# Kernel optimization log

Measured on AMD Instinct MI355X. Metric: run time of the kernel, lower is better.

The kernel has to match this reference:

```python
import jax, jax.numpy as jnp
import numpy as np

N = 50000      # nodes
E = 800000     # edges (avg degree 16)
D = 128        # node_dim
H = 128        # hidden_dim
ED = 16        # edge_dim (unused by GCNConv, kept for signature fidelity)
G = 64         # graphs in batch
EPS = 1e-5     # BatchNorm eps


def setup_inputs() -> dict:
    key = jax.random.key(0)
    ks = jax.random.split(key, 16)
    s = 0.05
    inp = {
        "x": jax.random.normal(ks[0], (N, D), jnp.float32),
        "edge_index": jax.random.randint(ks[1], (2, E), 0, N, dtype=jnp.int64),
        "edge_attr": jax.random.normal(ks[2], (E, ED), jnp.float32),
        "batch": jnp.sort(jax.random.randint(ks[3], (N,), 0, G, dtype=jnp.int64)),
        # GCNConv weights/biases
        "W1": jax.random.normal(ks[4], (D, H), jnp.float32) * s,
        "b1": jnp.zeros((H,), jnp.float32),
        "W2": jax.random.normal(ks[5], (H, H), jnp.float32) * s,
        "b2": jnp.zeros((H,), jnp.float32),
        "W3": jax.random.normal(ks[6], (H, H), jnp.float32) * s,
        "b3": jnp.zeros((H,), jnp.float32),
        # BatchNorm affine params (training-mode batch stats)
        "g1": jnp.ones((H,), jnp.float32), "be1": jnp.zeros((H,), jnp.float32),
        "g2": jnp.ones((H,), jnp.float32), "be2": jnp.zeros((H,), jnp.float32),
        "g3": jnp.ones((H,), jnp.float32), "be3": jnp.zeros((H,), jnp.float32),
    }
    return inp


def reference(x, edge_index, edge_attr, batch,
              W1, b1, W2, b2, W3, b3,
              g1, be1, g2, be2, g3, be3):
    n = x.shape[0]
    src, dst = edge_index[0], edge_index[1]

    # GCN symmetric normalization with added self-loops:
    # deg[i] = 1 + in_degree(i); norm(e) = deg[src]^-1/2 * deg[dst]^-1/2
    deg = jax.ops.segment_sum(jnp.ones((src.shape[0],), x.dtype), dst,
                              num_segments=n) + 1.0
    dinv = jax.lax.rsqrt(deg)
    edge_norm = (dinv[src] * dinv[dst])[:, None]   # [E,1]
    self_norm = (dinv * dinv)[:, None]             # [N,1] self-loop weight

    def gcn(h, W, b):
        h = h @ W                                  # [N,H]
        agg = jax.ops.segment_sum(h[src] * edge_norm, dst, num_segments=n)
        return agg + h * self_norm + b

    def bn_sigmoid(h, g, b):
        m = h.mean(0)
        v = jnp.mean(jnp.square(h - m), 0)         # biased variance (torch BN)
        return jax.nn.sigmoid((h - m) * jax.lax.rsqrt(v + EPS) * g + b)

    h = bn_sigmoid(gcn(x, W1, b1), g1, be1)
    h = bn_sigmoid(gcn(h, W2, b2), g2, be2)
    h = bn_sigmoid(gcn(h, W3, b3), g3, be3)

    # global_mean_pool over graph ids
    cnt = jax.ops.segment_sum(jnp.ones((n,), h.dtype), batch, num_segments=G)
    pooled = jax.ops.segment_sum(h, batch, num_segments=G)
    return pooled / jnp.maximum(cnt, 1.0)[:, None]
```

## Files before the change

kernel.cpp:

```cpp
#include <hip/hip_runtime.h>
#include <math.h>

#define NDIM 128

typedef __attribute__((ext_vector_type(8))) short short8;
typedef __attribute__((ext_vector_type(4))) float f32x4;

__device__ __forceinline__ float sigmoidf_(float x){ return 1.0f/(1.0f + __expf(-x)); }

__device__ __forceinline__ unsigned short f2bf(float f){
  unsigned u = __float_as_uint(f);
  unsigned r = (u + 0x7fffu + ((u >> 16) & 1u)) >> 16;
  return (unsigned short)r;
}
__device__ __forceinline__ float bflo(unsigned u){ return __uint_as_float(u<<16); }
__device__ __forceinline__ float bfhi(unsigned u){ return __uint_as_float(u & 0xffff0000u); }

__global__ void pass1_k(const int* __restrict__ dst, int* __restrict__ counts,
                        int* __restrict__ rank, int E){
  int e = blockIdx.x*blockDim.x + threadIdx.x;
  if(e < E) rank[e] = atomicAdd(&counts[dst[e]], 1);
}

__global__ void scan1_k(const int* __restrict__ counts, int* __restrict__ scanned,
                        int* __restrict__ chunksums, int N){
  __shared__ int lds[256];
  int t = threadIdx.x; int idx = blockIdx.x*256 + t;
  int x = (idx < N) ? counts[idx] : 0;
  lds[t] = x; __syncthreads();
  for(int o=1;o<256;o<<=1){
    int v = (t>=o) ? lds[t-o] : 0;
    __syncthreads();
    lds[t] += v;
    __syncthreads();
  }
  if(idx < N) scanned[idx] = lds[t];
  if(t == 255) chunksums[blockIdx.x] = lds[255];
}

__global__ void scan2_k(int* __restrict__ chunksums, int nchunks){
  __shared__ int lds[256];
  int t = threadIdx.x;
  int x = (t < nchunks) ? chunksums[t] : 0;
  lds[t] = x; __syncthreads();
  for(int o=1;o<256;o<<=1){
    int v = (t>=o) ? lds[t-o] : 0;
    __syncthreads();
    lds[t] += v;
    __syncthreads();
  }
  if(t < nchunks) chunksums[t] = lds[t] - x;
}

__global__ void scan3_k(const int* __restrict__ scanned, const int* __restrict__ counts,
                        const int* __restrict__ chunksums, int* __restrict__ row_start,
                        float* __restrict__ dinv, int N){
  int i = blockIdx.x*blockDim.x + threadIdx.x;
  if(i < N){
    row_start[i] = scanned[i] - counts[i] + chunksums[i>>8];
    dinv[i] = rsqrtf(1.0f + (float)counts[i]);
  }
}

__global__ void pass2_k(const int* __restrict__ src, const int* __restrict__ dst,
                        const int* __restrict__ rank, const int* __restrict__ row_start,
                        unsigned short* __restrict__ csr, int E){
  int e = blockIdx.x*blockDim.x + threadIdx.x;
  if(e >= E) return;
  csr[row_start[dst[e]] + rank[e]] = (unsigned short)src[e];
}

__global__ void wprep_k(const float* __restrict__ W0, const float* __restrict__ W1,
                        const float* __restrict__ W2, unsigned short* __restrict__ Wsw,
                        const int* __restrict__ batch, int* __restrict__ bound,
                        int N, int G){
  int t = blockIdx.x*256 + threadIdx.x;
  if(t < 3*16384){
    int l = t >> 14; int i = t & 16383;
    const float* W = (l==0) ? W0 : ((l==1) ? W1 : W2);
    int k = i >> 7, n = i & 127;
    Wsw[l*16384 + (((k>>3)*128 + n)<<3) + (k&7)] = f2bf(W[k*128+n]);
  } else {
    int g = t - 3*16384;
    if(g <= G){
      int lo = 0, hi = N;
      while(lo < hi){ int mid = (lo+hi)>>1; if(batch[mid] < g) lo = mid+1; else hi = mid; }
      bound[g] = lo;
    }
  }
}

__global__ __launch_bounds__(256) void gemm_mfma_k(const void* __restrict__ Avoid,
                                                   const unsigned short* __restrict__ Wsw,
                                                   unsigned short* __restrict__ Bh,
                                                   const float* __restrict__ dinv,
                                                   const float* __restrict__ sums,
                                                   const float* __restrict__ sumsq,
                                                   const float* __restrict__ gam,
                                                   const float* __restrict__ bet,
                                                   int N){
  __shared__ unsigned short Al[16384];
  __shared__ unsigned short Wl[16384];
  __shared__ float scl[NDIM], shl[NDIM], dvl[NDIM];
  int t = threadIdx.x;
  int row0 = blockIdx.x * 128;
  bool bn = (sums != nullptr);

  if(bn && t < NDIM){
    float invN = 1.0f/(float)N;
    float m = sums[t]*invN;
    float var = fmaxf(sumsq[t]*invN - m*m, 0.f);
    float s = gam[t]*rsqrtf(var + 1e-5f);
    scl[t] = s; shl[t] = bet[t] - m*s;
  }
  if(t < NDIM){
    int r = row0 + t;
    dvl[t] = (r < N) ? dinv[r] : 0.f;
  }
  #pragma unroll
  for(int i=0;i<8;i++){
    int u = t + i*256;
    *(uint4*)&Wl[u<<3] = *(const uint4*)&Wsw[u<<3];
  }
  __syncthreads();

  int o = t & 15, rbase = t >> 4;
  if(bn){
    const unsigned* Ab = (const unsigned*)Avoid;
    #pragma unroll
    for(int it=0; it<8; it++){
      int r = rbase + it*16;
      int grow = row0 + r;
      uint4 pk = {0,0,0,0};
      if(grow < N){
        uint4 pb = *(const uint4*)&Ab[(size_t)grow*64 + o*4];
        float a0=bflo(pb.x), a1=bfhi(pb.x), a2=bflo(pb.y), a3=bfhi(pb.y);
        float a4=bflo(pb.z), a5=bfhi(pb.z), a6=bflo(pb.w), a7=bfhi(pb.w);
        int f = o*8;
        a0 = sigmoidf_(a0*scl[f+0] + shl[f+0]);
        a1 = sigmoidf_(a1*scl[f+1] + shl[f+1]);
        a2 = sigmoidf_(a2*scl[f+2] + shl[f+2]);
        a3 = sigmoidf_(a3*scl[f+3] + shl[f+3]);
        a4 = sigmoidf_(a4*scl[f+4] + shl[f+4]);
        a5 = sigmoidf_(a5*scl[f+5] + shl[f+5]);
        a6 = sigmoidf_(a6*scl[f+6] + shl[f+6]);
        a7 = sigmoidf_(a7*scl[f+7] + shl[f+7]);
        pk.x = (unsigned)f2bf(a0) | ((unsigned)f2bf(a1)<<16);
        pk.y = (unsigned)f2bf(a2) | ((unsigned)f2bf(a3)<<16);
        pk.z = (unsigned)f2bf(a4) | ((unsigned)f2bf(a5)<<16);
        pk.w = (unsigned)f2bf(a6) | ((unsigned)f2bf(a7)<<16);
      }
      *(uint4*)&Al[(o*128 + r)<<3] = pk;
    }
  } else {
    const float* A = (const float*)Avoid;
    #pragma unroll
    for(int it=0; it<8; it++){
      int r = rbase + it*16;
      int grow = row0 + r;
      uint4 pk = {0,0,0,0};
      if(grow < N){
        float4 v0 = *(const float4*)&A[(size_t)grow*NDIM + o*8];
        float4 v1 = *(const float4*)&A[(size_t)grow*NDIM + o*8 + 4];
        pk.x = (unsigned)f2bf(v0.x) | ((unsigned)f2bf(v0.y)<<16);
        pk.y = (unsigned)f2bf(v0.z) | ((unsigned)f2bf(v0.w)<<16);
        pk.z = (unsigned)f2bf(v1.x) | ((unsigned)f2bf(v1.y)<<16);
        pk.w = (unsigned)f2bf(v1.z) | ((unsigned)f2bf(v1.w)<<16);
      }
      *(uint4*)&Al[(o*128 + r)<<3] = pk;
    }
  }
  __syncthreads();

  int wv = t >> 6, lane = t & 63, quad = lane >> 4, l16 = lane & 15;
  int rw = (wv & 1) * 64, cw = (wv >> 1) * 64;
  f32x4 acc[4][4];
  #pragma unroll
  for(int rt=0;rt<4;rt++)
    #pragma unroll
    for(int ct=0;ct<4;ct++) acc[rt][ct] = (f32x4){0.f,0.f,0.f,0.f};

  #pragma unroll
  for(int ks=0; ks<4; ks++){
    short8 a[4], b[4];
    #pragma unroll
    for(int rt=0;rt<4;rt++)
      a[rt] = *(short8*)&Al[(((ks*4+quad)*128) + rw + rt*16 + l16) << 3];
    #pragma unroll
    for(int ct=0;ct<4;ct++)
      b[ct] = *(short8*)&Wl[(((ks*4+quad)*128) + cw + ct*16 + l16) << 3];
    #pragma unroll
    for(int rt=0;rt<4;rt++)
      #pragma unroll
      for(int ct=0;ct<4;ct++)
        acc[rt][ct] = __builtin_amdgcn_mfma_f32_16x16x32_bf16(a[rt], b[ct], acc[rt][ct], 0, 0, 0);
  }

  #pragma unroll
  for(int rt=0;rt<4;rt++){
    int lr = rw + rt*16 + quad*4;
    int gr = row0 + lr;
    #pragma unroll
    for(int reg=0;reg<4;reg++){
      float dv = dvl[lr + reg];
      if(gr + reg < N){
        #pragma unroll
        for(int ct=0;ct<4;ct++){
          int col = cw + ct*16 + l16;
          Bh[(size_t)(gr+reg)*NDIM + col] = f2bf(acc[rt][ct][reg]*dv);
        }
      }
    }
  }
}

__global__ void agg_k(const unsigned int* __restrict__ hb,
                      const float* __restrict__ dinv,
                      const int* __restrict__ row_start, const int* __restrict__ counts,
                      const unsigned short* __restrict__ csr,
                      const float* __restrict__ bias, unsigned int* __restrict__ hCb, int N){
  int i = blockIdx.x;
  if(i >= N) return;
  int lane = threadIdx.x;
  int rs = row_start[i], re = rs + counts[i];
  float ax = 0.f, ay = 0.f;
  int j = rs;
  for(; j+7 < re; j += 8){
    int s0=csr[j],   s1=csr[j+1], s2=csr[j+2], s3=csr[j+3];
    int s4=csr[j+4], s5=csr[j+5], s6=csr[j+6], s7=csr[j+7];
    unsigned u0 = hb[(size_t)s0*64 + lane];
    unsigned u1 = hb[(size_t)s1*64 + lane];
    unsigned u2 = hb[(size_t)s2*64 + lane];
    unsigned u3 = hb[(size_t)s3*64 + lane];
    unsigned u4 = hb[(size_t)s4*64 + lane];
    unsigned u5 = hb[(size_t)s5*64 + lane];
    unsigned u6 = hb[(size_t)s6*64 + lane];
    unsigned u7 = hb[(size_t)s7*64 + lane];
    ax += bflo(u0)+bflo(u1)+bflo(u2)+bflo(u3)+bflo(u4)+bflo(u5)+bflo(u6)+bflo(u7);
    ay += bfhi(u0)+bfhi(u1)+bfhi(u2)+bfhi(u3)+bfhi(u4)+bfhi(u5)+bfhi(u6)+bfhi(u7);
  }
  for(; j < re; j++){
    unsigned u0 = hb[(size_t)csr[j]*64 + lane];
    ax += bflo(u0);
    ay += bfhi(u0);
  }
  float di = dinv[i];
  unsigned su = hb[(size_t)i*64 + lane];
  float2 bv = *(const float2*)&bias[lane*2];
  float ox = di*(ax + bflo(su)) + bv.x;
  float oy = di*(ay + bfhi(su)) + bv.y;
  hCb[(size_t)i*64 + lane] = (unsigned)f2bf(ox) | ((unsigned)f2bf(oy)<<16);
}

__global__ void stats_k(const unsigned* __restrict__ hb, float* __restrict__ sums,
                        float* __restrict__ sumsq, int N){
  __shared__ float ls[256], lq[256];
  int t = threadIdx.x;
  int f = t & 127, half = t >> 7;
  int rowsPerBlock = (N + gridDim.x - 1)/gridDim.x;
  int r0 = blockIdx.x * rowsPerBlock;
  int r1 = min(N, r0 + rowsPerBlock);
  float s=0.f, q=0.f;
  for(int r=r0+half; r<r1; r+=2){
    unsigned u = hb[(size_t)r*64 + (f>>1)];
    float v = (f&1) ? bfhi(u) : bflo(u);
    s += v; q += v*v;
  }
  ls[t]=s; lq[t]=q; __syncthreads();
  if(t < 128){
    s = ls[t] + ls[t+128];
    q = lq[t] + lq[t+128];
    atomicAdd(&sums[f], s);
    atomicAdd(&sumsq[f], q);
  }
}

#define PCH 128
__global__ __launch_bounds__(256) void pool_k(const unsigned* __restrict__ hb,
                                              const int* __restrict__ batch,
                                              const float* __restrict__ sums,
                                              const float* __restrict__ sumsq,
                                              const float* __restrict__ gam,
                                              const float* __restrict__ bet,
                                              float* __restrict__ out, int N){
  __shared__ float scl[NDIM], shl[NDIM];
  int t = threadIdx.x;
  if(t < NDIM){
    float invN = 1.0f/(float)N;
    float m = sums[t]*invN;
    float var = fmaxf(sumsq[t]*invN - m*m, 0.f);
    float s = gam[t]*rsqrtf(var + 1e-5f);
    scl[t] = s; shl[t] = bet[t] - m*s;
  }
  __syncthreads();
  int f = t & 127, half = t >> 7;
  int r0 = blockIdx.x*PCH + half;
  int r1 = min(N, blockIdx.x*PCH + PCH);
  float sc = scl[f], sh = shl[f];
  float acc = 0.f; int cur = -1;
  for(int r = r0; r < r1; r += 2){
    int g = batch[r];
    if(g != cur){
      if(cur >= 0) atomicAdd(&out[cur*NDIM + f], acc);
      acc = 0.f; cur = g;
    }
    unsigned u = hb[(size_t)r*64 + (f>>1)];
    float v = (f&1) ? bfhi(u) : bflo(u);
    acc += sigmoidf_(v*sc + sh);
  }
  if(cur >= 0) atomicAdd(&out[cur*NDIM + f], acc);
}

__global__ void div_k(float* __restrict__ out, const int* __restrict__ bound){
  int g = blockIdx.x, f = threadIdx.x;
  float cnt = (float)(bound[g+1] - bound[g]);
  out[g*NDIM + f] /= fmaxf(cnt, 1.0f);
}

extern "C" void kernel_launch(void* const* d_in, const int* in_sizes, int n_in,
                              void* d_out, int out_size, void* d_ws, size_t ws_size,
                              hipStream_t stream){
  const float* x     = (const float*)d_in[0];
  const int*   ei    = (const int*)d_in[1];
  const int*   batch = (const int*)d_in[3];
  const float* W [3] = {(const float*)d_in[4], (const float*)d_in[6], (const float*)d_in[8]};
  const float* bi[3] = {(const float*)d_in[5], (const float*)d_in[7], (const float*)d_in[9]};
  const float* gg[3] = {(const float*)d_in[10], (const float*)d_in[12], (const float*)d_in[14]};
  const float* bb[3] = {(const float*)d_in[11], (const float*)d_in[13], (const float*)d_in[15]};

  int N = in_sizes[0] / NDIM;
  int E = in_sizes[1] / 2;
  int G = out_size / NDIM;
  const int* src = ei;
  const int* dst = ei + E;

  char* p = (char*)d_ws;
  auto alloc = [&](size_t bytes)->void*{
    void* r = (void*)p; p += (bytes + 255) & ~(size_t)255; return r;
  };
  unsigned short* hB  = (unsigned short*)alloc((size_t)N*NDIM*2);
  unsigned*       hCb = (unsigned*)      alloc((size_t)N*64*4);
  unsigned short* Wsw = (unsigned short*)alloc(3*16384*2);
  int*   counts    = (int*)  alloc((size_t)N*4);
  int*   rank      = (int*)  alloc((size_t)E*4);
  int*   scanned   = (int*)  alloc((size_t)N*4);
  int*   chunksums = (int*)  alloc(256*4);
  int*   row_start = (int*)  alloc((size_t)N*4);
  float* dinv      = (float*)alloc((size_t)N*4);
  unsigned short* csr = (unsigned short*)alloc((size_t)E*2);
  float* sums      = (float*)alloc(2*3*128*4);
  float* sumsq     = sums + 3*128;
  int*   bound     = (int*)  alloc(256*4);

  hipMemsetAsync(counts, 0, (size_t)N*4, stream);
  hipMemsetAsync(sums,  0, 2*3*128*4, stream);
  hipMemsetAsync(d_out, 0, (size_t)out_size*4, stream);

  pass1_k<<<(E+255)/256, 256, 0, stream>>>(dst, counts, rank, E);

  int nchunks = (N+255)/256;
  scan1_k<<<nchunks, 256, 0, stream>>>(counts, scanned, chunksums, N);
  scan2_k<<<1, 256, 0, stream>>>(chunksums, nchunks);
  scan3_k<<<(N+255)/256, 256, 0, stream>>>(scanned, counts, chunksums, row_start, dinv, N);
  pass2_k<<<(E+255)/256, 256, 0, stream>>>(src, dst, rank, row_start, csr, E);
  wprep_k<<<(3*16384+256+255)/256, 256, 0, stream>>>(W[0], W[1], W[2], Wsw, batch, bound, N, G);

  const void* hin = (const void*)x;
  for(int l=0; l<3; l++){
    const float* sm = (l == 0) ? nullptr : (sums  + (l-1)*128);
    const float* sq = (l == 0) ? nullptr : (sumsq + (l-1)*128);
    const float* gm = (l == 0) ? nullptr : gg[l-1];
    const float* be = (l == 0) ? nullptr : bb[l-1];
    gemm_mfma_k<<<(N+127)/128, 256, 0, stream>>>(hin, Wsw + l*16384, hB, dinv,
                                                 sm, sq, gm, be, N);
    agg_k<<<N, 64, 0, stream>>>((const unsigned int*)hB, dinv, row_start, counts,
                                csr, bi[l], hCb, N);
    stats_k<<<400, 256, 0, stream>>>(hCb, sums + l*128, sumsq + l*128, N);
    hin = (const void*)hCb;
  }

  pool_k<<<(N+PCH-1)/PCH, 256, 0, stream>>>(hCb, batch, sums + 2*128, sumsq + 2*128,
                                            gg[2], bb[2], (float*)d_out, N);
  div_k<<<G, 128, 0, stream>>>((float*)d_out, bound);
}
```

Measured before the change: 448.9 us.

## Merge memsets into init kernel, fuse scan passes, pack four nodes per agg block

Three hipMemsetAsync calls become one init kernel. The single-block chunk-sum scan is folded into scan3, where each block rescans the chunk sums redundantly to find its own offset. The aggregation kernel now handles four nodes per 256-thread block, one wave each, instead of one 64-thread block per node. Together these cut launch count and per-block scheduling overhead, at the cost of some redundant scan work in every block.

```diff
diff --git a/kernel.cpp b/kernel.cpp
--- a/kernel.cpp
+++ b/kernel.cpp
@@ -15,6 +15,14 @@
 }
 __device__ __forceinline__ float bflo(unsigned u){ return __uint_as_float(u<<16); }
 __device__ __forceinline__ float bfhi(unsigned u){ return __uint_as_float(u & 0xffff0000u); }
+
+__global__ void init_k(int* __restrict__ counts, float* __restrict__ sums,
+                       float* __restrict__ out, int N, int outsz){
+  int i = blockIdx.x*256 + threadIdx.x;
+  if(i < N) counts[i] = 0;
+  if(i < 2*3*128) sums[i] = 0.f;
+  if(i < outsz) out[i] = 0.f;
+}
 
 __global__ void pass1_k(const int* __restrict__ dst, int* __restrict__ counts,
                         int* __restrict__ rank, int E){
@@ -38,9 +46,11 @@
   if(t == 255) chunksums[blockIdx.x] = lds[255];
 }
 
-__global__ void scan2_k(int* __restrict__ chunksums, int nchunks){
+__global__ void scan3_k(const int* __restrict__ scanned, const int* __restrict__ counts,
+                        const int* __restrict__ chunksums, int* __restrict__ row_start,
+                        float* __restrict__ dinv, int N, int nchunks){
   __shared__ int lds[256];
-  int t = threadIdx.x;
+  int t = threadIdx.x, b = blockIdx.x;
   int x = (t < nchunks) ? chunksums[t] : 0;
   lds[t] = x; __syncthreads();
   for(int o=1;o<256;o<<=1){
@@ -49,15 +59,10 @@
     lds[t] += v;
     __syncthreads();
   }
-  if(t < nchunks) chunksums[t] = lds[t] - x;
-}
-
-__global__ void scan3_k(const int* __restrict__ scanned, const int* __restrict__ counts,
-                        const int* __restrict__ chunksums, int* __restrict__ row_start,
-                        float* __restrict__ dinv, int N){
-  int i = blockIdx.x*blockDim.x + threadIdx.x;
+  int base = (b == 0) ? 0 : lds[b-1];
+  int i = b*256 + t;
   if(i < N){
-    row_start[i] = scanned[i] - counts[i] + chunksums[i>>8];
+    row_start[i] = scanned[i] - counts[i] + base;
     dinv[i] = rsqrtf(1.0f + (float)counts[i]);
   }
 }
@@ -214,14 +219,15 @@
   }
 }
 
-__global__ void agg_k(const unsigned int* __restrict__ hb,
+__global__ __launch_bounds__(256) void agg_k(const unsigned int* __restrict__ hb,
                       const float* __restrict__ dinv,
                       const int* __restrict__ row_start, const int* __restrict__ counts,
                       const unsigned short* __restrict__ csr,
                       const float* __restrict__ bias, unsigned int* __restrict__ hCb, int N){
-  int i = blockIdx.x;
+  int t = threadIdx.x;
+  int lane = t & 63;
+  int i = blockIdx.x*4 + (t >> 6);
   if(i >= N) return;
-  int lane = threadIdx.x;
   int rs = row_start[i], re = rs + counts[i];
   float ax = 0.f, ay = 0.f;
   int j = rs;
@@ -352,16 +358,14 @@
   float* sumsq     = sums + 3*128;
   int*   bound     = (int*)  alloc(256*4);
 
-  hipMemsetAsync(counts, 0, (size_t)N*4, stream);
-  hipMemsetAsync(sums,  0, 2*3*128*4, stream);
-  hipMemsetAsync(d_out, 0, (size_t)out_size*4, stream);
+  int initmax = (N > out_size) ? N : out_size;
+  init_k<<<(initmax+255)/256, 256, 0, stream>>>(counts, sums, (float*)d_out, N, out_size);
 
   pass1_k<<<(E+255)/256, 256, 0, stream>>>(dst, counts, rank, E);
 
   int nchunks = (N+255)/256;
   scan1_k<<<nchunks, 256, 0, stream>>>(counts, scanned, chunksums, N);
-  scan2_k<<<1, 256, 0, stream>>>(chunksums, nchunks);
-  scan3_k<<<(N+255)/256, 256, 0, stream>>>(scanned, counts, chunksums, row_start, dinv, N);
+  scan3_k<<<nchunks, 256, 0, stream>>>(scanned, counts, chunksums, row_start, dinv, N, nchunks);
   pass2_k<<<(E+255)/256, 256, 0, stream>>>(src, dst, rank, row_start, csr, E);
   wprep_k<<<(3*16384+256+255)/256, 256, 0, stream>>>(W[0], W[1], W[2], Wsw, batch, bound, N, G);
 
@@ -373,8 +377,8 @@
     const float* be = (l == 0) ? nullptr : bb[l-1];
     gemm_mfma_k<<<(N+127)/128, 256, 0, stream>>>(hin, Wsw + l*16384, hB, dinv,
                                                  sm, sq, gm, be, N);
-    agg_k<<<N, 64, 0, stream>>>((const unsigned int*)hB, dinv, row_start, counts,
-                                csr, bi[l], hCb, N);
+    agg_k<<<(N+3)/4, 256, 0, stream>>>((const unsigned int*)hB, dinv, row_start, counts,
+                                       csr, bi[l], hCb, N);
     stats_k<<<400, 256, 0, stream>>>(hCb, sums + l*128, sumsq + l*128, N);
     hin = (const void*)hCb;
   }
```

Result: slower. 458.7 us (+2.2%).
